# Kernel optimization log

Measured on AMD Instinct MI355X. Metric: run time of the kernel, lower is better.

Reference implementation:

```python
import jax, jax.numpy as jnp
import numpy as np


def setup_inputs() -> dict:
    key = jax.random.key(0)
    k0, k1, k2, k3 = jax.random.split(key, 4)
    B, C_IN, H, W = 8, 256, 64, 64
    O, NUM = 256, 8  # output channels, number of regions
    mat0 = jax.random.normal(k0, (B, C_IN, H, W), dtype=jnp.float32)
    mat1 = jax.random.normal(k1, (O, C_IN, NUM), dtype=jnp.float32)  # per-region 1x1 filters (shared across batch, batch_W=1)
    mask = jax.random.uniform(k2, (NUM, H, W), dtype=jnp.float32)    # soft region weights per pixel
    Alpha = jax.random.uniform(k3, (NUM,), dtype=jnp.float32)        # per-region modulation scale
    return {"mat0": mat0, "mat1": mat1, "mask": mask, "Alpha": Alpha, "use_alpha": 1, "beta": 1}


def reference(mat0, mat1, mask, Alpha, use_alpha, beta):
    # Deformable (region-aware) matmul: for each pixel (h,w), apply the
    # region-r filter mat1[:, :, r] to mat0[:, :, h, w], weighted by the
    # per-pixel soft region mask (optionally alpha-modulated per region).
    # out[b,o,h,w] = sum_r sum_c mat0[b,c,h,w] * mat1[o,c,r] * Alpha[r] * mask[r,h,w]
    m1 = mat1 * Alpha if use_alpha else mat1  # [O, C, R] scaled per region
    return jnp.einsum('bchw,ocr,rhw->bohw', mat0, m1, mask)
```

## Files before the change

kernel.cpp:

```cpp
#include <hip/hip_runtime.h>
#include <hip/hip_bf16.h>
#include <stdint.h>


typedef __attribute__((ext_vector_type(8)))  _Float16 half8;
typedef __attribute__((ext_vector_type(16))) float    f32x16;

#define C_IN  256
#define HW_   4096

__global__ __launch_bounds__(256) void prep_w_kernel(
    const float* __restrict__ mat1, const float* __restrict__ Alpha,
    const int* __restrict__ use_alpha, _Float16* __restrict__ Aprep) {
  int t = blockIdx.x * 256 + threadIdx.x;
  int o = t & 255;
  int c = t >> 8;
  int ua = use_alpha[0];
  const float* src = mat1 + ((size_t)o * C_IN + c) * 8;
  half8 v;
#pragma unroll
  for (int r = 0; r < 8; ++r) {
    float s = ua ? Alpha[r] : 1.0f;
    v[r] = (_Float16)(src[r] * s);
  }
  *(half8*)(Aprep + ((size_t)c * 256 + o) * 8) = v;
}

__global__ __launch_bounds__(512, 4) void gemm_deform_kernel(
    const float* __restrict__ mat0, const _Float16* __restrict__ Aprep,
    const float* __restrict__ mask, float* __restrict__ out) {
  __shared__ half8 A_lds[4][1024];

  int bid = blockIdx.x;
  int wg = (bid & 7) * 64 + (bid >> 3);
  int tile_m = wg & 1;
  int tile_n = wg >> 1;
  int o0 = tile_m * 128;
  int n0 = tile_n * 128;
  int b  = n0 >> 12;
  int p0 = n0 & 4095;

  int t    = threadIdx.x;
  int lane = t & 63;
  int w    = t >> 6;
  int wc   = w & 3;
  int wr   = w >> 2;
  int l31  = lane & 31;
  int cr   = lane >> 5;

  int colb = p0 + wc * 32 + l31;
  half8 mkh;
#pragma unroll
  for (int r = 0; r < 8; ++r) mkh[r] = (_Float16)mask[r * HW_ + colb];

  const __attribute__((address_space(1))) uint32_t* gA =
      (const __attribute__((address_space(1))) uint32_t*)Aprep;
  __attribute__((address_space(3))) uint32_t* lA =
      (__attribute__((address_space(3))) uint32_t*)&A_lds[0][0];
  int srow = t & 127;
  int scq  = t >> 7;
  const __attribute__((address_space(1))) uint32_t* gS0 =
      gA + (size_t)(scq * 256 + o0 + srow) * 4;
  const __attribute__((address_space(1))) uint32_t* gS1 =
      gA + (size_t)((4 + scq) * 256 + o0 + srow) * 4;
  const float* __restrict__ m0b =
      mat0 + ((size_t)b * C_IN + cr) * HW_ + colb;
  const float* pP0 = m0b + (size_t)0 * HW_;
  const float* pP1 = m0b + (size_t)2 * HW_;
  const float* pP2 = m0b + (size_t)4 * HW_;
  const float* pP3 = m0b + (size_t)6 * HW_;

#define STAGE(SLAB, SB) do {                                                  \
    __builtin_amdgcn_global_load_lds(gS0, lA + (size_t)((SLAB)*1024 + t) * 4,       16, 0, 0); \
    __builtin_amdgcn_global_load_lds(gS1, lA + (size_t)((SLAB)*1024 + 512 + t) * 4, 16, 0, 0); \
    gS0 += (SB); gS1 += (SB);                                                 \
  } while (0)

  f32x16 acc0, acc1;
#pragma unroll
  for (int j = 0; j < 16; ++j) { acc0[j] = 0.f; acc1[j] = 0.f; }

  float Pev[4], Pod[4];

  auto SM = [&](float s, half8 A0, half8 A1) {
    _Float16 h = (_Float16)s;
    half8 pb = {h, h, h, h, h, h, h, h};
    half8 bv = pb * mkh;
    acc0 = __builtin_amdgcn_mfma_f32_32x32x16_f16(A0, bv, acc0, 0, 0, 0);
    acc1 = __builtin_amdgcn_mfma_f32_32x32x16_f16(A1, bv, acc1, 0, 0, 0);
  };

  int abase = wr * 64 + l31;

  auto COMP = [&](const half8* __restrict__ Ab, float (&P)[4], int PB) {
    half8 a0 = Ab[(0 + cr) * 128 + abase];
    half8 a1 = Ab[(0 + cr) * 128 + abase + 32];
    half8 b0 = Ab[(2 + cr) * 128 + abase];
    half8 b1 = Ab[(2 + cr) * 128 + abase + 32];
    SM(P[0], a0, a1);
    P[0] = pP0[0]; pP0 += PB;
    a0 = Ab[(4 + cr) * 128 + abase];
    a1 = Ab[(4 + cr) * 128 + abase + 32];
    SM(P[1], b0, b1);
    P[1] = pP1[0]; pP1 += PB;
    b0 = Ab[(6 + cr) * 128 + abase];
    b1 = Ab[(6 + cr) * 128 + abase + 32];
    SM(P[2], a0, a1);
    P[2] = pP2[0]; pP2 += PB;
    SM(P[3], b0, b1);
    P[3] = pP3[0]; pP3 += PB;
  };

  STAGE(0, 8192);
  STAGE(1, 8192);
  Pev[0] = pP0[0]; pP0 += 8 * HW_;
  Pev[1] = pP1[0]; pP1 += 8 * HW_;
  Pev[2] = pP2[0]; pP2 += 8 * HW_;
  Pev[3] = pP3[0]; pP3 += 8 * HW_;
  Pod[0] = pP0[0]; pP0 += 8 * HW_;
  Pod[1] = pP1[0]; pP1 += 8 * HW_;
  Pod[2] = pP2[0]; pP2 += 8 * HW_;
  Pod[3] = pP3[0]; pP3 += 8 * HW_;

#pragma unroll 1
  for (int g = 0; g < 8; ++g) {
    int rd = g * 4;
    asm volatile("s_waitcnt vmcnt(8)" ::: "memory");
    __builtin_amdgcn_s_barrier();
    {
      int sb2 = (rd + 2 < 31) ? 8192 : 0;
      int sb3 = (rd + 3 < 31) ? 8192 : 0;
      int pb2 = (rd + 2 < 31) ? 8 * HW_ : 0;
      int pb3 = (rd + 3 < 31) ? 8 * HW_ : 0;
      STAGE(2, sb2);
      STAGE(3, sb3);
      COMP(&A_lds[0][0], Pev, pb2);
      COMP(&A_lds[1][0], Pod, pb3);
    }
    asm volatile("s_waitcnt vmcnt(8)" ::: "memory");
    __builtin_amdgcn_s_barrier();
    {
      int sb4 = (rd + 4 < 31) ? 8192 : 0;
      int sb5 = (rd + 5 < 31) ? 8192 : 0;
      int pb4 = (rd + 4 < 31) ? 8 * HW_ : 0;
      int pb5 = (rd + 5 < 31) ? 8 * HW_ : 0;
      STAGE(0, sb4);
      STAGE(1, sb5);
      COMP(&A_lds[2][0], Pev, pb4);
      COMP(&A_lds[3][0], Pod, pb5);
    }
  }

  size_t obase = (size_t)b * 256 * HW_ + colb;
#pragma unroll
  for (int reg = 0; reg < 16; ++reg) {
    int row = o0 + wr * 64 + (reg & 3) + 8 * (reg >> 2) + 4 * cr;
    out[obase + (size_t)row * HW_]        = acc0[reg];
    out[obase + (size_t)(row + 32) * HW_] = acc1[reg];
  }
}

extern "C" void kernel_launch(void* const* d_in, const int* in_sizes, int n_in,
                              void* d_out, int out_size, void* d_ws, size_t ws_size,
                              hipStream_t stream) {
  const float* mat0      = (const float*)d_in[0];
  const float* mat1      = (const float*)d_in[1];
  const float* mask      = (const float*)d_in[2];
  const float* Alpha     = (const float*)d_in[3];
  const int*   use_alpha = (const int*)d_in[4];
  (void)in_sizes; (void)n_in; (void)out_size; (void)ws_size;

  _Float16* Aprep = (_Float16*)d_ws;
  float* outp  = (float*)d_out;

  prep_w_kernel<<<256, 256, 0, stream>>>(mat1, Alpha, use_alpha, Aprep);
  gemm_deform_kernel<<<512, 512, 0, stream>>>(mat0, Aprep, mask, outp);
}
```

Measured before the change: 48.81 us.

## Halve workgroup to 4 waves, each computing 32x128 tile with 4 MFMA column blocks

The GEMM workgroup shrinks from 8 to 4 waves, and each wave now owns 32 output rows across all 128 columns (four 32x32 accumulators) instead of a 64x32 block. Each A fragment read from LDS is reused across four MFMAs, and each lane loads four mat0 values per channel. The staging copy now issues four LDS-direct loads per thread to fill the same slabs. The waits become vmcnt(0), which serialises the A prefetch more strictly. Fewer threads per block and more registers per thread also lower occupancy and latency hiding for the strided mat0 loads.

After: 51.99 us. 6.5% more time.

```diff
diff --git a/kernel.cpp b/kernel.cpp
--- a/kernel.cpp
+++ b/kernel.cpp
@@ -26,7 +26,7 @@
   *(half8*)(Aprep + ((size_t)c * 256 + o) * 8) = v;
 }
 
-__global__ __launch_bounds__(512, 4) void gemm_deform_kernel(
+__global__ __launch_bounds__(256, 2) void gemm_deform_kernel(
     const float* __restrict__ mat0, const _Float16* __restrict__ Aprep,
     const float* __restrict__ mask, float* __restrict__ out) {
   __shared__ half8 A_lds[4][1024];
@@ -43,26 +43,32 @@
   int t    = threadIdx.x;
   int lane = t & 63;
   int w    = t >> 6;
-  int wc   = w & 3;
-  int wr   = w >> 2;
   int l31  = lane & 31;
   int cr   = lane >> 5;
 
-  int colb = p0 + wc * 32 + l31;
-  half8 mkh;
+  int colb = p0 + l31;
+  half8 mkh[4];
 #pragma unroll
-  for (int r = 0; r < 8; ++r) mkh[r] = (_Float16)mask[r * HW_ + colb];
+  for (int nc = 0; nc < 4; ++nc)
+#pragma unroll
+    for (int r = 0; r < 8; ++r)
+      mkh[nc][r] = (_Float16)mask[r * HW_ + colb + nc * 32];
 
   const __attribute__((address_space(1))) uint32_t* gA =
       (const __attribute__((address_space(1))) uint32_t*)Aprep;
   __attribute__((address_space(3))) uint32_t* lA =
       (__attribute__((address_space(3))) uint32_t*)&A_lds[0][0];
+  int scq  = t >> 7;
   int srow = t & 127;
-  int scq  = t >> 7;
   const __attribute__((address_space(1))) uint32_t* gS0 =
-      gA + (size_t)(scq * 256 + o0 + srow) * 4;
+      gA + (size_t)((0 + scq) * 256 + o0 + srow) * 4;
   const __attribute__((address_space(1))) uint32_t* gS1 =
+      gA + (size_t)((2 + scq) * 256 + o0 + srow) * 4;
+  const __attribute__((address_space(1))) uint32_t* gS2 =
       gA + (size_t)((4 + scq) * 256 + o0 + srow) * 4;
+  const __attribute__((address_space(1))) uint32_t* gS3 =
+      gA + (size_t)((6 + scq) * 256 + o0 + srow) * 4;
+
   const float* __restrict__ m0b =
       mat0 + ((size_t)b * C_IN + cr) * HW_ + colb;
   const float* pP0 = m0b + (size_t)0 * HW_;
@@ -72,60 +78,68 @@
 
 #define STAGE(SLAB, SB) do {                                                  \
     __builtin_amdgcn_global_load_lds(gS0, lA + (size_t)((SLAB)*1024 + t) * 4,       16, 0, 0); \
-    __builtin_amdgcn_global_load_lds(gS1, lA + (size_t)((SLAB)*1024 + 512 + t) * 4, 16, 0, 0); \
-    gS0 += (SB); gS1 += (SB);                                                 \
+    __builtin_amdgcn_global_load_lds(gS1, lA + (size_t)((SLAB)*1024 + 256 + t) * 4, 16, 0, 0); \
+    __builtin_amdgcn_global_load_lds(gS2, lA + (size_t)((SLAB)*1024 + 512 + t) * 4, 16, 0, 0); \
+    __builtin_amdgcn_global_load_lds(gS3, lA + (size_t)((SLAB)*1024 + 768 + t) * 4, 16, 0, 0); \
+    gS0 += (SB); gS1 += (SB); gS2 += (SB); gS3 += (SB);                       \
   } while (0)
 
-  f32x16 acc0, acc1;
+  f32x16 acc[4];
 #pragma unroll
-  for (int j = 0; j < 16; ++j) { acc0[j] = 0.f; acc1[j] = 0.f; }
+  for (int nc = 0; nc < 4; ++nc)
+#pragma unroll
+    for (int j = 0; j < 16; ++j) acc[nc][j] = 0.f;
 
-  float Pev[4], Pod[4];
+  float Pev[4][4], Pod[4][4];
 
-  auto SM = [&](float s, half8 A0, half8 A1) {
-    _Float16 h = (_Float16)s;
-    half8 pb = {h, h, h, h, h, h, h, h};
-    half8 bv = pb * mkh;
-    acc0 = __builtin_amdgcn_mfma_f32_32x32x16_f16(A0, bv, acc0, 0, 0, 0);
-    acc1 = __builtin_amdgcn_mfma_f32_32x32x16_f16(A1, bv, acc1, 0, 0, 0);
+  auto SMk = [&](const float (&Pk)[4], half8 A) {
+#pragma unroll
+    for (int nc = 0; nc < 4; ++nc) {
+      _Float16 h = (_Float16)Pk[nc];
+      half8 pb = {h, h, h, h, h, h, h, h};
+      half8 bv = pb * mkh[nc];
+      acc[nc] = __builtin_amdgcn_mfma_f32_32x32x16_f16(A, bv, acc[nc], 0, 0, 0);
+    }
   };
 
-  int abase = wr * 64 + l31;
+  int abase = w * 32 + l31;
 
-  auto COMP = [&](const half8* __restrict__ Ab, float (&P)[4], int PB) {
+  auto COMP = [&](const half8* __restrict__ Ab, float (&P)[4][4], int PB) {
     half8 a0 = Ab[(0 + cr) * 128 + abase];
-    half8 a1 = Ab[(0 + cr) * 128 + abase + 32];
-    half8 b0 = Ab[(2 + cr) * 128 + abase];
-    half8 b1 = Ab[(2 + cr) * 128 + abase + 32];
-    SM(P[0], a0, a1);
-    P[0] = pP0[0]; pP0 += PB;
+    half8 a1 = Ab[(2 + cr) * 128 + abase];
+    SMk(P[0], a0);
+    P[0][0] = pP0[0]; P[0][1] = pP0[32]; P[0][2] = pP0[64]; P[0][3] = pP0[96];
+    pP0 += PB;
     a0 = Ab[(4 + cr) * 128 + abase];
-    a1 = Ab[(4 + cr) * 128 + abase + 32];
-    SM(P[1], b0, b1);
-    P[1] = pP1[0]; pP1 += PB;
-    b0 = Ab[(6 + cr) * 128 + abase];
-    b1 = Ab[(6 + cr) * 128 + abase + 32];
-    SM(P[2], a0, a1);
-    P[2] = pP2[0]; pP2 += PB;
-    SM(P[3], b0, b1);
-    P[3] = pP3[0]; pP3 += PB;
+    SMk(P[1], a1);
+    P[1][0] = pP1[0]; P[1][1] = pP1[32]; P[1][2] = pP1[64]; P[1][3] = pP1[96];
+    pP1 += PB;
+    a1 = Ab[(6 + cr) * 128 + abase];
+    SMk(P[2], a0);
+    P[2][0] = pP2[0]; P[2][1] = pP2[32]; P[2][2] = pP2[64]; P[2][3] = pP2[96];
+    pP2 += PB;
+    SMk(P[3], a1);
+    P[3][0] = pP3[0]; P[3][1] = pP3[32]; P[3][2] = pP3[64]; P[3][3] = pP3[96];
+    pP3 += PB;
+  };
+
+  auto LOADP = [&](float (&P)[4][4]) {
+    P[0][0] = pP0[0]; P[0][1] = pP0[32]; P[0][2] = pP0[64]; P[0][3] = pP0[96];
+    P[1][0] = pP1[0]; P[1][1] = pP1[32]; P[1][2] = pP1[64]; P[1][3] = pP1[96];
+    P[2][0] = pP2[0]; P[2][1] = pP2[32]; P[2][2] = pP2[64]; P[2][3] = pP2[96];
+    P[3][0] = pP3[0]; P[3][1] = pP3[32]; P[3][2] = pP3[64]; P[3][3] = pP3[96];
+    pP0 += 8 * HW_; pP1 += 8 * HW_; pP2 += 8 * HW_; pP3 += 8 * HW_;
   };
 
   STAGE(0, 8192);
   STAGE(1, 8192);
-  Pev[0] = pP0[0]; pP0 += 8 * HW_;
-  Pev[1] = pP1[0]; pP1 += 8 * HW_;
-  Pev[2] = pP2[0]; pP2 += 8 * HW_;
-  Pev[3] = pP3[0]; pP3 += 8 * HW_;
-  Pod[0] = pP0[0]; pP0 += 8 * HW_;
-  Pod[1] = pP1[0]; pP1 += 8 * HW_;
-  Pod[2] = pP2[0]; pP2 += 8 * HW_;
-  Pod[3] = pP3[0]; pP3 += 8 * HW_;
+  LOADP(Pev);
+  LOADP(Pod);
 
 #pragma unroll 1
   for (int g = 0; g < 8; ++g) {
     int rd = g * 4;
-    asm volatile("s_waitcnt vmcnt(8)" ::: "memory");
+    asm volatile("s_waitcnt vmcnt(0)" ::: "memory");
     __builtin_amdgcn_s_barrier();
     {
       int sb2 = (rd + 2 < 31) ? 8192 : 0;
@@ -137,7 +151,7 @@
       COMP(&A_lds[0][0], Pev, pb2);
       COMP(&A_lds[1][0], Pod, pb3);
     }
-    asm volatile("s_waitcnt vmcnt(8)" ::: "memory");
+    asm volatile("s_waitcnt vmcnt(0)" ::: "memory");
     __builtin_amdgcn_s_barrier();
     {
       int sb4 = (rd + 4 < 31) ? 8192 : 0;
@@ -153,10 +167,12 @@
 
   size_t obase = (size_t)b * 256 * HW_ + colb;
 #pragma unroll
-  for (int reg = 0; reg < 16; ++reg) {
-    int row = o0 + wr * 64 + (reg & 3) + 8 * (reg >> 2) + 4 * cr;
-    out[obase + (size_t)row * HW_]        = acc0[reg];
-    out[obase + (size_t)(row + 32) * HW_] = acc1[reg];
+  for (int nc = 0; nc < 4; ++nc) {
+#pragma unroll
+    for (int reg = 0; reg < 16; ++reg) {
+      int row = o0 + w * 32 + (reg & 3) + 8 * (reg >> 2) + 4 * cr;
+      out[obase + (size_t)row * HW_ + nc * 32] = acc[nc][reg];
+    }
   }
 }
 
@@ -174,5 +190,5 @@
   float* outp  = (float*)d_out;
 
   prep_w_kernel<<<256, 256, 0, stream>>>(mat1, Alpha, use_alpha, Aprep);
-  gemm_deform_kernel<<<512, 512, 0, stream>>>(mat0, Aprep, mask, outp);
+  gemm_deform_kernel<<<512, 256, 0, stream>>>(mat0, Aprep, mask, outp);
 }
```
